# Kernel tuning notes

Measured on AMD Instinct MI355X. Metric: run time of the kernel, lower is better.

The kernel has to match this reference:

```python
import jax, jax.numpy as jnp
import numpy as np

B, N, D, H, C = 4, 1024, 768, 12, 3
Dh = D // H                      # 64
HID = int(D * 4.0 * (2.0 / 3.0)) # 2048 (SwiGLU hidden)
EPS = 1e-5


def layernorm(x, g, b):
    m = jnp.mean(x, axis=-1, keepdims=True)
    v = jnp.mean(jnp.square(x - m), axis=-1, keepdims=True)
    return (x - m) * jax.lax.rsqrt(v + EPS) * g + b


def setup_inputs() -> dict:
    key = jax.random.key(0)
    ks = jax.random.split(key, 8)
    x = jax.random.normal(ks[0], (B, N, D), jnp.float32)
    coords = jax.random.uniform(ks[1], (B, N, C), jnp.float32)
    qkv_w = jax.random.normal(ks[2], (3 * D, D), jnp.float32) * 0.02
    qkv_b = jnp.zeros((3 * D,), jnp.float32)
    rel_w = jax.random.normal(ks[3], (H, C), jnp.float32) * 0.1
    ln1_g = jnp.ones((D,), jnp.float32)
    ln1_b = jnp.zeros((D,), jnp.float32)
    ln2_g = jnp.ones((D,), jnp.float32)
    ln2_b = jnp.zeros((D,), jnp.float32)
    win_w = jax.random.normal(ks[4], (2 * HID, D), jnp.float32) * 0.02
    win_b = jnp.zeros((2 * HID,), jnp.float32)
    wout_w = jax.random.normal(ks[5], (D, HID), jnp.float32) * 0.02
    wout_b = jnp.zeros((D,), jnp.float32)
    return dict(x=x, coords=coords, ln1_g=ln1_g, ln1_b=ln1_b, qkv_w=qkv_w,
                qkv_b=qkv_b, rel_w=rel_w, ln2_g=ln2_g, ln2_b=ln2_b,
                win_w=win_w, win_b=win_b, wout_w=wout_w, wout_b=wout_b)


def reference(x, coords, ln1_g, ln1_b, qkv_w, qkv_b, rel_w, ln2_g, ln2_b,
              win_w, win_b, wout_w, wout_b):
    # --- PatchAttention on norm1(x) ---
    h = layernorm(x, ln1_g, ln1_b)
    qkv = h @ qkv_w.T + qkv_b                    # (B,N,3D)
    q, k, v = jnp.split(qkv, 3, axis=-1)

    def heads(t):  # (B,N,D) -> (B,H,N,Dh)
        return t.reshape(B, N, H, Dh).transpose(0, 2, 1, 3)

    qh, kh, vh = heads(q), heads(k), heads(v)
    scale = 1.0 / np.sqrt(Dh).astype(np.float32)
    scores = jnp.einsum('bhid,bhjd->bhij', qh, kh) * scale
    # coord bias: (coords_i - coords_j) . W_h  ==  p[b,h,i] - p[b,h,j]
    p = jnp.einsum('bnc,hc->bhn', coords, rel_w)  # (B,H,N)
    scores = scores + p[:, :, :, None] - p[:, :, None, :]
    attn = jax.nn.softmax(scores, axis=-1)
    o = jnp.einsum('bhij,bhjd->bhid', attn, vh)   # (B,H,N,Dh)
    o = o.transpose(0, 2, 1, 3).reshape(B, N, D)
    x = x + o

    # --- SwiGLU FFN on norm2(x) ---
    h2 = layernorm(x, ln2_g, ln2_b)
    uv = h2 @ win_w.T + win_b                     # (B,N,2*HID)
    u, g = jnp.split(uv, 2, axis=-1)
    act = jax.nn.silu(u) * g
    return x + act @ wout_w.T + wout_b
```

## Files before the change

kernel.cpp:

```cpp
#include <hip/hip_runtime.h>
#include <math.h>

typedef unsigned short u16;
typedef __bf16 bf16x8 __attribute__((ext_vector_type(8)));
typedef __bf16 bf16x4 __attribute__((ext_vector_type(4)));
typedef u16 u16x4 __attribute__((ext_vector_type(4)));
typedef float f32x4 __attribute__((ext_vector_type(4)));

#define NTOK 1024
#define DMODEL 768
#define NHEAD 12
#define LD3 2304
#define HIDDIM 2048

__device__ __forceinline__ float b2f(u16 u) {
  unsigned int t = ((unsigned int)u) << 16;
  float f;
  __builtin_memcpy(&f, &t, 4);
  return f;
}
__device__ __forceinline__ u16 f2b(float f) {
  unsigned int t;
  __builtin_memcpy(&t, &f, 4);
  t += 0x7fffu + ((t >> 16) & 1u);
  return (u16)(t >> 16);
}

__device__ __forceinline__ void gl_lds16(const u16* g, u16* l) {
  __builtin_amdgcn_global_load_lds(
      (__attribute__((address_space(1))) const unsigned int*)g,
      (__attribute__((address_space(3))) unsigned int*)l, 16, 0, 0);
}

__global__ __launch_bounds__(256) void signal_kernel(float* __restrict__ out,
                                                     int n, float c) {
  int i = blockIdx.x * 256 + threadIdx.x;
  if (i < n) out[i] = c;
}

struct CanonJobs {
  const void* s[13];
  u16* d[13];
  int n[13];
};

__global__ __launch_bounds__(256) void canon_kernel(CanonJobs jobs) {
  __shared__ int csh;
  u16 v = ((const u16*)jobs.s[0])[2 * threadIdx.x];
  int e = (v >> 7) & 0xFF;
  unsigned long long m = __ballot(e >= 0xC0);
  if (threadIdx.x == 0) csh = 0;
  __syncthreads();
  if ((threadIdx.x & 63) == 0) atomicAdd(&csh, __popcll(m));
  __syncthreads();
  bool isf32 = csh >= 8;

  int j = blockIdx.y;
  int n4 = jobs.n[j] >> 2;
  const void* s = jobs.s[j];
  u16* d = jobs.d[j];
  for (int i = blockIdx.x * 256 + threadIdx.x; i < n4; i += gridDim.x * 256) {
    if (isf32) {
      f32x4 vv = *((const f32x4*)s + i);
      u16x4 o = {f2b(vv[0]), f2b(vv[1]), f2b(vv[2]), f2b(vv[3])};
      *((u16x4*)d + i) = o;
    } else {
      *((u16x4*)d + i) = *((const u16x4*)s + i);
    }
  }
}

__global__ __launch_bounds__(256) void ln_bf16_kernel(
    const u16* __restrict__ x, const u16* __restrict__ g,
    const u16* __restrict__ b, u16* __restrict__ out) {
  int row = blockIdx.x;
  int tid = threadIdx.x;
  const u16* xr = x + (size_t)row * DMODEL;
  float v0 = b2f(xr[tid]), v1 = b2f(xr[tid + 256]), v2 = b2f(xr[tid + 512]);
  float s = v0 + v1 + v2;
  float q = v0 * v0 + v1 * v1 + v2 * v2;
#pragma unroll
  for (int off = 32; off; off >>= 1) {
    s += __shfl_xor(s, off, 64);
    q += __shfl_xor(q, off, 64);
  }
  __shared__ float rs[4], rq[4];
  int wv = tid >> 6;
  if ((tid & 63) == 0) { rs[wv] = s; rq[wv] = q; }
  __syncthreads();
  s = rs[0] + rs[1] + rs[2] + rs[3];
  q = rq[0] + rq[1] + rq[2] + rq[3];
  float mean = s * (1.0f / 768.0f);
  float var = q * (1.0f / 768.0f) - mean * mean;
  float inv = rsqrtf(var + 1e-5f);
  u16* outr = out + (size_t)row * DMODEL;
  outr[tid]       = f2b((v0 - mean) * inv * b2f(g[tid])       + b2f(b[tid]));
  outr[tid + 256] = f2b((v1 - mean) * inv * b2f(g[tid + 256]) + b2f(b[tid + 256]));
  outr[tid + 512] = f2b((v2 - mean) * inv * b2f(g[tid + 512]) + b2f(b[tid + 512]));
}

__global__ __launch_bounds__(256) void ln_f32_kernel(
    const float* __restrict__ x, const u16* __restrict__ g,
    const u16* __restrict__ b, u16* __restrict__ out) {
  int row = blockIdx.x;
  int tid = threadIdx.x;
  const float* xr = x + (size_t)row * DMODEL;
  float v0 = xr[tid], v1 = xr[tid + 256], v2 = xr[tid + 512];
  float s = v0 + v1 + v2;
  float q = v0 * v0 + v1 * v1 + v2 * v2;
#pragma unroll
  for (int off = 32; off; off >>= 1) {
    s += __shfl_xor(s, off, 64);
    q += __shfl_xor(q, off, 64);
  }
  __shared__ float rs[4], rq[4];
  int wv = tid >> 6;
  if ((tid & 63) == 0) { rs[wv] = s; rq[wv] = q; }
  __syncthreads();
  s = rs[0] + rs[1] + rs[2] + rs[3];
  q = rq[0] + rq[1] + rq[2] + rq[3];
  float mean = s * (1.0f / 768.0f);
  float var = q * (1.0f / 768.0f) - mean * mean;
  float inv = rsqrtf(var + 1e-5f);
  u16* outr = out + (size_t)row * DMODEL;
  outr[tid]       = f2b((v0 - mean) * inv * b2f(g[tid])       + b2f(b[tid]));
  outr[tid + 256] = f2b((v1 - mean) * inv * b2f(g[tid + 256]) + b2f(b[tid + 256]));
  outr[tid + 512] = f2b((v2 - mean) * inv * b2f(g[tid + 512]) + b2f(b[tid + 512]));
}

__global__ __launch_bounds__(256) void gemm_bt(
    const u16* __restrict__ Ap, const u16* __restrict__ Wp,
    const u16* __restrict__ bias, u16* __restrict__ Cp, int Nn, int K) {
  __shared__ __align__(16) u16 Al[3 * 128 * 32], Bl[3 * 64 * 32];
  int lane = threadIdx.x & 63;
  int wv = threadIdx.x >> 6;
  int q16 = lane & 15, quad = lane >> 4;
  int mB0 = blockIdx.y * 128;
  int nB0 = blockIdx.x * 64;
  int mW = (wv >> 1) * 64, nW = (wv & 1) * 32;
  int srow = lane >> 2;
  int scol = ((lane & 3) ^ ((lane >> 3) & 3)) * 8;
  int sx8 = (quad ^ ((q16 >> 1) & 3)) * 8;
  int r0 = wv * 32 + srow, r1 = r0 + 16;
  int rb = wv * 16 + srow;
  const u16* Ag0 = Ap + (size_t)(mB0 + r0) * K + scol;
  const u16* Ag1 = Ap + (size_t)(mB0 + r1) * K + scol;
  const u16* Wg  = Wp + (size_t)(nB0 + rb) * K + scol;
  int ch0 = wv * 1024, ch1 = ch0 + 512, chb = wv * 512;
  int nsteps = K >> 5;
  f32x4 acc[4][2] = {};
#pragma unroll
  for (int tt = 0; tt < 2; ++tt) {
    int k0 = tt * 32;
    gl_lds16(Ag0 + k0, Al + tt * 4096 + ch0);
    gl_lds16(Ag1 + k0, Al + tt * 4096 + ch1);
    gl_lds16(Wg + k0, Bl + tt * 2048 + chb);
  }
  int n3 = nsteps / 3;
  for (int kb = 0; kb < n3; ++kb) {
#pragma unroll
    for (int c = 0; c < 3; ++c) {
      int t = kb * 3 + c;
      if (t < nsteps - 1) asm volatile("s_waitcnt vmcnt(3)" ::: "memory");
      else                asm volatile("s_waitcnt vmcnt(0)" ::: "memory");
      __builtin_amdgcn_sched_barrier(0);
      __builtin_amdgcn_s_barrier();
      __builtin_amdgcn_sched_barrier(0);
      if (t < nsteps - 2) {
        int k0 = (t + 2) * 32;
        int bs = (c + 2) % 3;
        gl_lds16(Ag0 + k0, Al + bs * 4096 + ch0);
        gl_lds16(Ag1 + k0, Al + bs * 4096 + ch1);
        gl_lds16(Wg + k0, Bl + bs * 2048 + chb);
      }
      const __bf16* Ab = (const __bf16*)(Al + c * 4096);
      const __bf16* Bb = (const __bf16*)(Bl + c * 2048);
      bf16x8 af[4], bfr[2];
#pragma unroll
      for (int si = 0; si < 4; ++si)
        af[si] = *(const bf16x8*)(Ab + (mW + si * 16 + q16) * 32 + sx8);
#pragma unroll
      for (int sj = 0; sj < 2; ++sj)
        bfr[sj] = *(const bf16x8*)(Bb + (nW + sj * 16 + q16) * 32 + sx8);
#pragma unroll
      for (int si = 0; si < 4; ++si)
#pragma unroll
        for (int sj = 0; sj < 2; ++sj)
          acc[si][sj] = __builtin_amdgcn_mfma_f32_16x16x32_bf16(af[si], bfr[sj], acc[si][sj], 0, 0, 0);
    }
  }
#pragma unroll
  for (int si = 0; si < 4; ++si)
#pragma unroll
    for (int sj = 0; sj < 2; ++sj) {
      int col = nB0 + nW + sj * 16 + q16;
      float bcol = b2f(bias[col]);
#pragma unroll
      for (int r = 0; r < 4; ++r) {
        int rowi = mB0 + mW + si * 16 + quad * 4 + r;
        Cp[(size_t)rowi * Nn + col] = f2b(acc[si][sj][r] + bcol);
      }
    }
}

__global__ __launch_bounds__(256) void gemm_out_f32(
    const u16* __restrict__ Ap, const u16* __restrict__ Wp,
    const u16* __restrict__ bias, const float* __restrict__ res,
    float* __restrict__ out) {
  __shared__ __align__(16) u16 Al[4 * 64 * 32], Bl[4 * 64 * 32];
  int lane = threadIdx.x & 63;
  int wv = threadIdx.x >> 6;
  int q16 = lane & 15, quad = lane >> 4;
  int mB0 = blockIdx.y * 64;
  int nB0 = blockIdx.x * 64;
  int mW = (wv >> 1) * 32, nW = (wv & 1) * 32;
  int srow = lane >> 2;
  int scol = ((lane & 3) ^ ((lane >> 3) & 3)) * 8;
  int sx8 = (quad ^ ((q16 >> 1) & 3)) * 8;
  int ra = wv * 16 + srow;
  const u16* Ag = Ap + (size_t)(mB0 + ra) * 2048 + scol;
  const u16* Wg = Wp + (size_t)(nB0 + ra) * 2048 + scol;
  int ch = wv * 512;
  f32x4 acc[2][2] = {};
#pragma unroll
  for (int tt = 0; tt < 3; ++tt) {
    gl_lds16(Ag + tt * 32, Al + tt * 2048 + ch);
    gl_lds16(Wg + tt * 32, Bl + tt * 2048 + ch);
  }
  for (int kb = 0; kb < 16; ++kb) {
#pragma unroll
    for (int c = 0; c < 4; ++c) {
      int t = kb * 4 + c;
      if (t < 62)       asm volatile("s_waitcnt vmcnt(4)" ::: "memory");
      else if (t == 62) asm volatile("s_waitcnt vmcnt(2)" ::: "memory");
      else              asm volatile("s_waitcnt vmcnt(0)" ::: "memory");
      __builtin_amdgcn_sched_barrier(0);
      __builtin_amdgcn_s_barrier();
      __builtin_amdgcn_sched_barrier(0);
      if (t < 61) {
        int k0 = (t + 3) * 32;
        int bs = (c + 3) & 3;
        gl_lds16(Ag + k0, Al + bs * 2048 + ch);
        gl_lds16(Wg + k0, Bl + bs * 2048 + ch);
      }
      const __bf16* Ab = (const __bf16*)(Al + c * 2048);
      const __bf16* Bb = (const __bf16*)(Bl + c * 2048);
      bf16x8 af[2], bfr[2];
#pragma unroll
      for (int si = 0; si < 2; ++si)
        af[si] = *(const bf16x8*)(Ab + (mW + si * 16 + q16) * 32 + sx8);
#pragma unroll
      for (int sj = 0; sj < 2; ++sj)
        bfr[sj] = *(const bf16x8*)(Bb + (nW + sj * 16 + q16) * 32 + sx8);
#pragma unroll
      for (int si = 0; si < 2; ++si)
#pragma unroll
        for (int sj = 0; sj < 2; ++sj)
          acc[si][sj] = __builtin_amdgcn_mfma_f32_16x16x32_bf16(af[si], bfr[sj], acc[si][sj], 0, 0, 0);
    }
  }
#pragma unroll
  for (int si = 0; si < 2; ++si)
#pragma unroll
    for (int sj = 0; sj < 2; ++sj) {
      int col = nB0 + nW + sj * 16 + q16;
      float bcol = b2f(bias[col]);
#pragma unroll
      for (int r = 0; r < 4; ++r) {
        int rowi = mB0 + mW + si * 16 + quad * 4 + r;
        size_t idx = (size_t)rowi * 768 + col;
        out[idx] = acc[si][sj][r] + bcol + res[idx];
      }
    }
}

__global__ __launch_bounds__(256) void ffn_in_kernel(
    const u16* __restrict__ hp, const u16* __restrict__ Wp,
    const u16* __restrict__ bias, u16* __restrict__ actp) {
  __shared__ __align__(16) u16 Al[6 * 128 * 32], Bl[6 * 64 * 32];
  int lane = threadIdx.x & 63;
  int wv = threadIdx.x >> 6;
  int q16 = lane & 15, quad = lane >> 4;
  int mB0 = blockIdx.y * 128;
  int cB0 = blockIdx.x * 32;
  int mW = (wv >> 1) * 64;
  int cW = (wv & 1) * 16;
  int srow = lane >> 2;
  int scol = ((lane & 3) ^ ((lane >> 3) & 3)) * 8;
  int sx8 = (quad ^ ((q16 >> 1) & 3)) * 8;
  int r0 = wv * 32 + srow, r1 = r0 + 16;
  int rb = wv * 16 + srow;
  int gb = (rb < 32) ? (cB0 + rb) : (HIDDIM + cB0 + rb - 32);
  const u16* Ag0 = hp + (size_t)(mB0 + r0) * DMODEL + scol;
  const u16* Ag1 = hp + (size_t)(mB0 + r1) * DMODEL + scol;
  const u16* Wg  = Wp + (size_t)gb * DMODEL + scol;
  int ch0 = wv * 1024, ch1 = ch0 + 512, chb = wv * 512;
  f32x4 au[4] = {}, ag[4] = {};
#pragma unroll
  for (int tt = 0; tt < 5; ++tt) {
    int k0 = tt * 32;
    gl_lds16(Ag0 + k0, Al + tt * 4096 + ch0);
    gl_lds16(Ag1 + k0, Al + tt * 4096 + ch1);
    gl_lds16(Wg + k0, Bl + tt * 2048 + chb);
  }
  for (int kb = 0; kb < 4; ++kb) {
#pragma unroll
    for (int c = 0; c < 6; ++c) {
      int t = kb * 6 + c;
      if (t < 20)       asm volatile("s_waitcnt vmcnt(12)" ::: "memory");
      else if (t == 20) asm volatile("s_waitcnt vmcnt(9)" ::: "memory");
      else if (t == 21) asm volatile("s_waitcnt vmcnt(6)" ::: "memory");
      else if (t == 22) asm volatile("s_waitcnt vmcnt(3)" ::: "memory");
      else              asm volatile("s_waitcnt vmcnt(0)" ::: "memory");
      __builtin_amdgcn_sched_barrier(0);
      __builtin_amdgcn_s_barrier();
      __builtin_amdgcn_sched_barrier(0);
      if (t < 19) {
        int k0 = (t + 5) * 32;
        int bs = (c + 5) % 6;
        gl_lds16(Ag0 + k0, Al + bs * 4096 + ch0);
        gl_lds16(Ag1 + k0, Al + bs * 4096 + ch1);
        gl_lds16(Wg + k0, Bl + bs * 2048 + chb);
      }
      const __bf16* Ab = (const __bf16*)(Al + c * 4096);
      const __bf16* Bb = (const __bf16*)(Bl + c * 2048);
      bf16x8 af[4], wu, wg;
#pragma unroll
      for (int si = 0; si < 4; ++si)
        af[si] = *(const bf16x8*)(Ab + (mW + si * 16 + q16) * 32 + sx8);
      wu = *(const bf16x8*)(Bb + (cW + q16) * 32 + sx8);
      wg = *(const bf16x8*)(Bb + (32 + cW + q16) * 32 + sx8);
#pragma unroll
      for (int si = 0; si < 4; ++si) {
        au[si] = __builtin_amdgcn_mfma_f32_16x16x32_bf16(af[si], wu, au[si], 0, 0, 0);
        ag[si] = __builtin_amdgcn_mfma_f32_16x16x32_bf16(af[si], wg, ag[si], 0, 0, 0);
      }
    }
  }
  int col = cB0 + cW + q16;
  float bu = b2f(bias[col]);
  float bg = b2f(bias[HIDDIM + col]);
#pragma unroll
  for (int si = 0; si < 4; ++si) {
#pragma unroll
    for (int r = 0; r < 4; ++r) {
      int rowi = mB0 + mW + si * 16 + quad * 4 + r;
      float u = au[si][r] + bu;
      float g = ag[si][r] + bg;
      float s = u / (1.0f + __expf(-u));
      actp[(size_t)rowi * HIDDIM + col] = f2b(s * g);
    }
  }
}

__global__ __launch_bounds__(256) void vt_kernel(const u16* __restrict__ qkvp,
                                                 u16* __restrict__ vtp,
                                                 const u16* __restrict__ coords,
                                                 const u16* __restrict__ relw,
                                                 float* __restrict__ p) {
  int blk = blockIdx.x;
  int b = blk / 192;
  int rem = blk % 192;
  int h = rem >> 4;
  int nt = rem & 15;
  int wv = threadIdx.x >> 6;
  int d = threadIdx.x & 63;
  int n0 = nt * 64 + wv * 16;
  const u16* src = qkvp + ((size_t)(b * NTOK) + n0) * LD3 + 2 * DMODEL + h * 64 + d;
  u16* dst = vtp + ((size_t)((b * NHEAD + h) * 64 + d)) * NTOK + n0;
#pragma unroll
  for (int c = 0; c < 2; ++c) {
    u16 buf[8] __attribute__((aligned(16)));
#pragma unroll
    for (int i = 0; i < 8; ++i) buf[i] = src[(size_t)(c * 8 + i) * LD3];
    *(uint4*)(dst + c * 8) = *(const uint4*)buf;
  }
  if (nt == 0) {
    const float LOG2E = 1.4426950408889634f;
    float w0 = b2f(relw[h * 3 + 0]), w1 = b2f(relw[h * 3 + 1]), w2 = b2f(relw[h * 3 + 2]);
    float* prow = p + (size_t)(b * NHEAD + h) * NTOK;
    for (int n = threadIdx.x; n < NTOK; n += 256) {
      int idx = b * NTOK + n;
      float c0 = b2f(coords[idx * 3 + 0]);
      float c1 = b2f(coords[idx * 3 + 1]);
      float c2 = b2f(coords[idx * 3 + 2]);
      prow[n] = (c0 * w0 + c1 * w1 + c2 * w2) * LOG2E;
    }
  }
}

__global__ __launch_bounds__(256) void attn_kernel(
    const u16* __restrict__ qkvp, const u16* __restrict__ vtp,
    const float* __restrict__ p2, const u16* __restrict__ xp,
    float* __restrict__ x1) {
  const __bf16* qb = (const __bf16*)qkvp;
  __shared__ __align__(16) u16 Kl[4][32 * 64];
  __shared__ __align__(16) u16 Vl[4][64 * 32];
  __shared__ __align__(16) u16 Pl[4][16][40];
  __shared__ __align__(16) float Pb[1024];
  int lane = threadIdx.x & 63;
  int wv = threadIdx.x >> 6;
  int hw = blockIdx.x;
  int g = hw % 48;
  int nt = hw / 48;
  int b = g / 12, h = g % 12;
  int i0 = (nt * 4 + wv) * 16;
  int q16 = lane & 15, quad = lane >> 4;

  const float scl2 = 0.125f * 1.4426950408889634f;

  const __bf16* qrow = qb + ((size_t)(b * NTOK) + i0 + q16) * LD3 + h * 64;
  bf16x8 bq0 = *(const bf16x8*)(qrow + quad * 8);
  bf16x8 bq1 = *(const bf16x8*)(qrow + 32 + quad * 8);

  const float* prow = p2 + (size_t)(b * NHEAD + h) * NTOK;

  int krw = wv * 8 + (lane >> 3);
  int ks  = (lane & 7) ^ (krw & 7);
  const u16* kg0 = qkvp + (size_t)(b * NTOK) * LD3 + DMODEL + h * 64 + ks * 8;
  int vrw = wv * 16 + (lane >> 2);
  int vs  = (lane & 3) ^ ((vrw >> 1) & 3);
  const u16* vg0 = vtp + ((size_t)((b * NHEAD + h) * 64 + vrw)) * NTOK + vs * 8;

  int kx0 = (quad ^ (q16 & 7)) << 3;
  int kx1 = ((4 | quad) ^ (q16 & 7)) << 3;
  int vx  = (quad ^ ((q16 >> 1) & 3)) << 3;

  float mrun = -1e30f, lsum = 0.f;
  f32x4 accO[4] = {};

  gl_lds16((const u16*)(prow + wv * 256 + lane * 4), (u16*)&Pb[wv * 256]);
#pragma unroll
  for (int tt = 0; tt < 3; ++tt) {
    gl_lds16(kg0 + (size_t)(tt * 32 + krw) * LD3, &Kl[tt][wv * 512]);
    gl_lds16(vg0 + tt * 32, &Vl[tt][wv * 512]);
  }

  for (int kb = 0; kb < 8; ++kb) {
#pragma unroll
    for (int c = 0; c < 4; ++c) {
      int t = kb * 4 + c;
      if (t < 30)       asm volatile("s_waitcnt vmcnt(4)" ::: "memory");
      else if (t == 30) asm volatile("s_waitcnt vmcnt(2)" ::: "memory");
      else              asm volatile("s_waitcnt vmcnt(0)" ::: "memory");
      __builtin_amdgcn_sched_barrier(0);
      __builtin_amdgcn_s_barrier();
      __builtin_amdgcn_sched_barrier(0);
      if (t < 29) {
        int j = (t + 3) * 32;
        gl_lds16(kg0 + (size_t)(j + krw) * LD3, &Kl[(c + 3) & 3][wv * 512]);
        gl_lds16(vg0 + j, &Vl[(c + 3) & 3][wv * 512]);
      }

      int j0 = t * 32;
      const __bf16* Kb = (const __bf16*)Kl[c];
      bf16x8 ka00 = *(const bf16x8*)(Kb + q16 * 64 + kx0);
      bf16x8 ka01 = *(const bf16x8*)(Kb + q16 * 64 + kx1);
      bf16x8 ka10 = *(const bf16x8*)(Kb + (16 + q16) * 64 + kx0);
      bf16x8 ka11 = *(const bf16x8*)(Kb + (16 + q16) * 64 + kx1);
      f32x4 st0 = {}, st1 = {};
      st0 = __builtin_amdgcn_mfma_f32_16x16x32_bf16(ka00, bq0, st0, 0, 0, 0);
      st0 = __builtin_amdgcn_mfma_f32_16x16x32_bf16(ka01, bq1, st0, 0, 0, 0);
      st1 = __builtin_amdgcn_mfma_f32_16x16x32_bf16(ka10, bq0, st1, 0, 0, 0);
      st1 = __builtin_amdgcn_mfma_f32_16x16x32_bf16(ka11, bq1, st1, 0, 0, 0);

      f32x4 pjl = *(const f32x4*)(&Pb[j0 + 4 * quad]);
      f32x4 pjh = *(const f32x4*)(&Pb[j0 + 16 + 4 * quad]);
      float sl[4], sh[4];
#pragma unroll
      for (int r = 0; r < 4; ++r) {
        sl[r] = st0[r] * scl2 - pjl[r];
        sh[r] = st1[r] * scl2 - pjh[r];
      }
      float lm = fmaxf(fmaxf(fmaxf(sl[0], sl[1]), fmaxf(sl[2], sl[3])),
                       fmaxf(fmaxf(sh[0], sh[1]), fmaxf(sh[2], sh[3])));
      lm = fmaxf(lm, __shfl_xor(lm, 16, 64));
      lm = fmaxf(lm, __shfl_xor(lm, 32, 64));
      float mn = fmaxf(mrun, lm);
      float alpha = exp2f(mrun - mn);
      mrun = mn;
      float pl[4], ph[4];
#pragma unroll
      for (int r = 0; r < 4; ++r) {
        pl[r] = exp2f(sl[r] - mn);
        ph[r] = exp2f(sh[r] - mn);
      }
      float ts = (pl[0] + pl[1]) + (pl[2] + pl[3]) +
                 (ph[0] + ph[1]) + (ph[2] + ph[3]);
      ts += __shfl_xor(ts, 16, 64);
      ts += __shfl_xor(ts, 32, 64);
      lsum = lsum * alpha + ts;

      bf16x4 w0 = {(__bf16)pl[0], (__bf16)pl[1], (__bf16)pl[2], (__bf16)pl[3]};
      bf16x4 w1 = {(__bf16)ph[0], (__bf16)ph[1], (__bf16)ph[2], (__bf16)ph[3]};
      *(bf16x4*)(&Pl[wv][q16][4 * quad]) = w0;
      *(bf16x4*)(&Pl[wv][q16][16 + 4 * quad]) = w1;
      bf16x8 ap = *(const bf16x8*)(&Pl[wv][q16][quad * 8]);

      const __bf16* Vb = (const __bf16*)Vl[c];
#pragma unroll
      for (int ds = 0; ds < 4; ++ds) {
        bf16x8 av = *(const bf16x8*)(Vb + (ds * 16 + q16) * 32 + vx);
        f32x4 cc = accO[ds];
#pragma unroll
        for (int r = 0; r < 4; ++r) cc[r] *= alpha;
        accO[ds] = __builtin_amdgcn_mfma_f32_16x16x32_bf16(av, ap, cc, 0, 0, 0);
      }
    }
  }

  float rl = 1.0f / lsum;
  size_t rowbase = ((size_t)(b * NTOK) + i0 + q16) * DMODEL + h * 64;
#pragma unroll
  for (int ds = 0; ds < 4; ++ds) {
    int d0 = ds * 16 + quad * 4;
    u16x4 xv = *(const u16x4*)(xp + rowbase + d0);
    f32x4 ov;
#pragma unroll
    for (int r = 0; r < 4; ++r) ov[r] = b2f(xv[r]) + accO[ds][r] * rl;
    *(f32x4*)(x1 + rowbase + d0) = ov;
  }
}

extern "C" void kernel_launch(void* const* d_in, const int* in_sizes, int n_in,
                              void* d_out, int out_size, void* d_ws, size_t ws_size,
                              hipStream_t stream) {
  static const int esz[13] = {3145728, 12288, 768, 768, 1769472, 2304, 36,
                              768, 768, 3145728, 4096, 1572864, 768};
  float sig = -1.f;
  if (n_in != 13) {
    sig = 6000.f + 100.f * (float)n_in;
  } else {
    for (int i = 0; i < 13; ++i)
      if (in_sizes[i] != esz[i]) { sig = 1000.f + 100.f * (float)i; break; }
  }
  if (sig < 0.f && ws_size < 57258496ULL) sig = 3000.f;
  if (sig < 0.f && out_size != 3145728) sig = 3100.f;
  if (sig >= 0.f) {
    signal_kernel<<<(out_size + 255) / 256, 256, 0, stream>>>((float*)d_out, out_size, sig);
    return;
  }

  char* ws = (char*)d_ws;
  u16*  cx      = (u16*)(ws + 256);
  u16*  cqkvw   = (u16*)(ws + 6291712);
  u16*  cwinw   = (u16*)(ws + 9830656);
  u16*  cwoutw  = (u16*)(ws + 16122112);
  u16*  ccoords = (u16*)(ws + 19267840);
  u16*  cln1g   = (u16*)(ws + 19292416);
  u16*  cln1b   = (u16*)(ws + 19293952);
  u16*  cqkvb   = (u16*)(ws + 19295488);
  u16*  crelw   = (u16*)(ws + 19300096);
  u16*  cln2g   = (u16*)(ws + 19300352);
  u16*  cln2b   = (u16*)(ws + 19301888);
  u16*  cwinb   = (u16*)(ws + 19303424);
  u16*  cwoutb  = (u16*)(ws + 19311616);
  u16*  h       = (u16*)(ws + 19313152);
  u16*  qkv     = (u16*)(ws + 25604608);
  float* pbuf   = (float*)(ws + 44478976);
  float* x1     = (float*)(ws + 44675584);
  u16*  act     = qkv;
  u16*  vt      = h;

  CanonJobs jobs;
  u16* dsts[13] = {cx, ccoords, cln1g, cln1b, cqkvw, cqkvb, crelw,
                   cln2g, cln2b, cwinw, cwinb, cwoutw, cwoutb};
  for (int i = 0; i < 13; ++i) {
    jobs.s[i] = d_in[i];
    jobs.d[i] = dsts[i];
    jobs.n[i] = in_sizes[i];
  }
  canon_kernel<<<dim3(768, 13), 256, 0, stream>>>(jobs);

  ln_bf16_kernel<<<4096, 256, 0, stream>>>(cx, cln1g, cln1b, h);
  gemm_bt<<<dim3(36, 32), 256, 0, stream>>>(h, cqkvw, cqkvb, qkv, 2304, 768);
  vt_kernel<<<768, 256, 0, stream>>>(qkv, vt, ccoords, crelw, pbuf);
  attn_kernel<<<768, 256, 0, stream>>>(qkv, vt, pbuf, cx, x1);
  ln_f32_kernel<<<4096, 256, 0, stream>>>(x1, cln2g, cln2b, h);
  ffn_in_kernel<<<dim3(64, 32), 256, 0, stream>>>(h, cwinw, cwinb, act);
  gemm_out_f32<<<dim3(12, 64), 256, 0, stream>>>(act, cwoutw, cwoutb, x1,
                                                 (float*)d_out);
}
```

Measured before the change: 287.2 us.

## Switch FFN GEMMs to double-buffered 64-wide K tiles and skip redundant softmax rescale

The output and FFN-input GEMMs drop their 4- and 6-stage 32-wide K pipelines in favour of two buffers of 64-wide K tiles with a new XOR swizzle. Each stage now waits for all loads to finish (vmcnt(0)) before its barrier. This halves the number of barriers and loop iterations, but it reduces prefetch depth and so hides less memory latency. The attention kernel adds a wave-uniform check and skips the running-max exp and accumulator rescale when no lane's max increases.

New measurement: 275.3 us. 4.1% less time.

```diff
diff --git a/kernel.cpp b/kernel.cpp
--- a/kernel.cpp
+++ b/kernel.cpp
@@ -207,56 +207,63 @@
     const u16* __restrict__ Ap, const u16* __restrict__ Wp,
     const u16* __restrict__ bias, const float* __restrict__ res,
     float* __restrict__ out) {
-  __shared__ __align__(16) u16 Al[4 * 64 * 32], Bl[4 * 64 * 32];
+  __shared__ __align__(16) u16 Al[2 * 4096], Bl[2 * 4096];
   int lane = threadIdx.x & 63;
   int wv = threadIdx.x >> 6;
   int q16 = lane & 15, quad = lane >> 4;
   int mB0 = blockIdx.y * 64;
   int nB0 = blockIdx.x * 64;
   int mW = (wv >> 1) * 32, nW = (wv & 1) * 32;
-  int srow = lane >> 2;
-  int scol = ((lane & 3) ^ ((lane >> 3) & 3)) * 8;
-  int sx8 = (quad ^ ((q16 >> 1) & 3)) * 8;
-  int ra = wv * 16 + srow;
-  const u16* Ag = Ap + (size_t)(mB0 + ra) * 2048 + scol;
-  const u16* Wg = Wp + (size_t)(nB0 + ra) * 2048 + scol;
-  int ch = wv * 512;
+  int lr = lane >> 3, ls = lane & 7;
+  int sg = (ls ^ lr) * 8;
+  int sx0 = (quad ^ (q16 & 7)) * 8;
+  int sx1 = ((4 | quad) ^ (q16 & 7)) * 8;
+  const u16* Ag = Ap + (size_t)(mB0 + wv * 16 + lr) * 2048 + sg;
+  const u16* Wg = Wp + (size_t)(nB0 + wv * 16 + lr) * 2048 + sg;
+  int ch = wv * 1024;
   f32x4 acc[2][2] = {};
 #pragma unroll
-  for (int tt = 0; tt < 3; ++tt) {
-    gl_lds16(Ag + tt * 32, Al + tt * 2048 + ch);
-    gl_lds16(Wg + tt * 32, Bl + tt * 2048 + ch);
+  for (int i = 0; i < 2; ++i) {
+    gl_lds16(Ag + (size_t)i * 8 * 2048, Al + ch + i * 512);
+    gl_lds16(Wg + (size_t)i * 8 * 2048, Bl + ch + i * 512);
   }
   for (int kb = 0; kb < 16; ++kb) {
 #pragma unroll
-    for (int c = 0; c < 4; ++c) {
-      int t = kb * 4 + c;
-      if (t < 62)       asm volatile("s_waitcnt vmcnt(4)" ::: "memory");
-      else if (t == 62) asm volatile("s_waitcnt vmcnt(2)" ::: "memory");
-      else              asm volatile("s_waitcnt vmcnt(0)" ::: "memory");
+    for (int c = 0; c < 2; ++c) {
+      int t = kb * 2 + c;
+      asm volatile("s_waitcnt vmcnt(0)" ::: "memory");
       __builtin_amdgcn_sched_barrier(0);
       __builtin_amdgcn_s_barrier();
       __builtin_amdgcn_sched_barrier(0);
-      if (t < 61) {
-        int k0 = (t + 3) * 32;
-        int bs = (c + 3) & 3;
-        gl_lds16(Ag + k0, Al + bs * 2048 + ch);
-        gl_lds16(Wg + k0, Bl + bs * 2048 + ch);
-      }
-      const __bf16* Ab = (const __bf16*)(Al + c * 2048);
-      const __bf16* Bb = (const __bf16*)(Bl + c * 2048);
-      bf16x8 af[2], bfr[2];
+      if (t < 31) {
+        int k0 = (t + 1) * 64;
+        int bs = c ^ 1;
+#pragma unroll
+        for (int i = 0; i < 2; ++i) {
+          gl_lds16(Ag + (size_t)i * 8 * 2048 + k0, Al + bs * 4096 + ch + i * 512);
+          gl_lds16(Wg + (size_t)i * 8 * 2048 + k0, Bl + bs * 4096 + ch + i * 512);
+        }
+      }
+      const __bf16* Ab = (const __bf16*)(Al + c * 4096);
+      const __bf16* Bb = (const __bf16*)(Bl + c * 4096);
+      bf16x8 a0[2], a1[2], b0[2], b1[2];
+#pragma unroll
+      for (int si = 0; si < 2; ++si) {
+        a0[si] = *(const bf16x8*)(Ab + (mW + si * 16 + q16) * 64 + sx0);
+        a1[si] = *(const bf16x8*)(Ab + (mW + si * 16 + q16) * 64 + sx1);
+      }
+#pragma unroll
+      for (int sj = 0; sj < 2; ++sj) {
+        b0[sj] = *(const bf16x8*)(Bb + (nW + sj * 16 + q16) * 64 + sx0);
+        b1[sj] = *(const bf16x8*)(Bb + (nW + sj * 16 + q16) * 64 + sx1);
+      }
 #pragma unroll
       for (int si = 0; si < 2; ++si)
-        af[si] = *(const bf16x8*)(Ab + (mW + si * 16 + q16) * 32 + sx8);
-#pragma unroll
-      for (int sj = 0; sj < 2; ++sj)
-        bfr[sj] = *(const bf16x8*)(Bb + (nW + sj * 16 + q16) * 32 + sx8);
-#pragma unroll
-      for (int si = 0; si < 2; ++si)
-#pragma unroll
-        for (int sj = 0; sj < 2; ++sj)
-          acc[si][sj] = __builtin_amdgcn_mfma_f32_16x16x32_bf16(af[si], bfr[sj], acc[si][sj], 0, 0, 0);
+#pragma unroll
+        for (int sj = 0; sj < 2; ++sj) {
+          acc[si][sj] = __builtin_amdgcn_mfma_f32_16x16x32_bf16(a0[si], b0[sj], acc[si][sj], 0, 0, 0);
+          acc[si][sj] = __builtin_amdgcn_mfma_f32_16x16x32_bf16(a1[si], b1[sj], acc[si][sj], 0, 0, 0);
+        }
     }
   }
 #pragma unroll
@@ -277,7 +284,7 @@
 __global__ __launch_bounds__(256) void ffn_in_kernel(
     const u16* __restrict__ hp, const u16* __restrict__ Wp,
     const u16* __restrict__ bias, u16* __restrict__ actp) {
-  __shared__ __align__(16) u16 Al[6 * 128 * 32], Bl[6 * 64 * 32];
+  __shared__ __align__(16) u16 Al[2 * 8192], Bl[2 * 4096];
   int lane = threadIdx.x & 63;
   int wv = threadIdx.x >> 6;
   int q16 = lane & 15, quad = lane >> 4;
@@ -285,55 +292,61 @@
   int cB0 = blockIdx.x * 32;
   int mW = (wv >> 1) * 64;
   int cW = (wv & 1) * 16;
-  int srow = lane >> 2;
-  int scol = ((lane & 3) ^ ((lane >> 3) & 3)) * 8;
-  int sx8 = (quad ^ ((q16 >> 1) & 3)) * 8;
-  int r0 = wv * 32 + srow, r1 = r0 + 16;
-  int rb = wv * 16 + srow;
-  int gb = (rb < 32) ? (cB0 + rb) : (HIDDIM + cB0 + rb - 32);
-  const u16* Ag0 = hp + (size_t)(mB0 + r0) * DMODEL + scol;
-  const u16* Ag1 = hp + (size_t)(mB0 + r1) * DMODEL + scol;
-  const u16* Wg  = Wp + (size_t)gb * DMODEL + scol;
-  int ch0 = wv * 1024, ch1 = ch0 + 512, chb = wv * 512;
+  int lr = lane >> 3, ls = lane & 7;
+  int sg = (ls ^ lr) * 8;
+  int sx0 = (quad ^ (q16 & 7)) * 8;
+  int sx1 = ((4 | quad) ^ (q16 & 7)) * 8;
+  const u16* Ag = hp + (size_t)(mB0 + wv * 32 + lr) * DMODEL + sg;
+  int rB0 = wv * 16 + lr, rB1 = rB0 + 8;
+  int gb0 = (rB0 < 32) ? (cB0 + rB0) : (HIDDIM + cB0 + rB0 - 32);
+  int gb1 = (rB1 < 32) ? (cB0 + rB1) : (HIDDIM + cB0 + rB1 - 32);
+  const u16* Wg0 = Wp + (size_t)gb0 * DMODEL + sg;
+  const u16* Wg1 = Wp + (size_t)gb1 * DMODEL + sg;
+  int chA = wv * 2048, chB = wv * 1024;
   f32x4 au[4] = {}, ag[4] = {};
 #pragma unroll
-  for (int tt = 0; tt < 5; ++tt) {
-    int k0 = tt * 32;
-    gl_lds16(Ag0 + k0, Al + tt * 4096 + ch0);
-    gl_lds16(Ag1 + k0, Al + tt * 4096 + ch1);
-    gl_lds16(Wg + k0, Bl + tt * 2048 + chb);
-  }
-  for (int kb = 0; kb < 4; ++kb) {
-#pragma unroll
-    for (int c = 0; c < 6; ++c) {
-      int t = kb * 6 + c;
-      if (t < 20)       asm volatile("s_waitcnt vmcnt(12)" ::: "memory");
-      else if (t == 20) asm volatile("s_waitcnt vmcnt(9)" ::: "memory");
-      else if (t == 21) asm volatile("s_waitcnt vmcnt(6)" ::: "memory");
-      else if (t == 22) asm volatile("s_waitcnt vmcnt(3)" ::: "memory");
-      else              asm volatile("s_waitcnt vmcnt(0)" ::: "memory");
+  for (int i = 0; i < 4; ++i)
+    gl_lds16(Ag + (size_t)i * 8 * DMODEL, Al + chA + i * 512);
+  gl_lds16(Wg0, Bl + chB);
+  gl_lds16(Wg1, Bl + chB + 512);
+  for (int kb = 0; kb < 6; ++kb) {
+#pragma unroll
+    for (int c = 0; c < 2; ++c) {
+      int t = kb * 2 + c;
+      asm volatile("s_waitcnt vmcnt(0)" ::: "memory");
       __builtin_amdgcn_sched_barrier(0);
       __builtin_amdgcn_s_barrier();
       __builtin_amdgcn_sched_barrier(0);
-      if (t < 19) {
-        int k0 = (t + 5) * 32;
-        int bs = (c + 5) % 6;
-        gl_lds16(Ag0 + k0, Al + bs * 4096 + ch0);
-        gl_lds16(Ag1 + k0, Al + bs * 4096 + ch1);
-        gl_lds16(Wg + k0, Bl + bs * 2048 + chb);
-      }
-      const __bf16* Ab = (const __bf16*)(Al + c * 4096);
-      const __bf16* Bb = (const __bf16*)(Bl + c * 2048);
-      bf16x8 af[4], wu, wg;
-#pragma unroll
-      for (int si = 0; si < 4; ++si)
-        af[si] = *(const bf16x8*)(Ab + (mW + si * 16 + q16) * 32 + sx8);
-      wu = *(const bf16x8*)(Bb + (cW + q16) * 32 + sx8);
-      wg = *(const bf16x8*)(Bb + (32 + cW + q16) * 32 + sx8);
+      if (t < 11) {
+        int k0 = (t + 1) * 64;
+        int bs = c ^ 1;
+#pragma unroll
+        for (int i = 0; i < 4; ++i)
+          gl_lds16(Ag + (size_t)i * 8 * DMODEL + k0, Al + bs * 8192 + chA + i * 512);
+        gl_lds16(Wg0 + k0, Bl + bs * 4096 + chB);
+        gl_lds16(Wg1 + k0, Bl + bs * 4096 + chB + 512);
+      }
+      const __bf16* Ab = (const __bf16*)(Al + c * 8192);
+      const __bf16* Bb = (const __bf16*)(Bl + c * 4096);
+      bf16x8 a0[4], a1[4];
 #pragma unroll
       for (int si = 0; si < 4; ++si) {
-        au[si] = __builtin_amdgcn_mfma_f32_16x16x32_bf16(af[si], wu, au[si], 0, 0, 0);
-        ag[si] = __builtin_amdgcn_mfma_f32_16x16x32_bf16(af[si], wg, ag[si], 0, 0, 0);
+        a0[si] = *(const bf16x8*)(Ab + (mW + si * 16 + q16) * 64 + sx0);
+        a1[si] = *(const bf16x8*)(Ab + (mW + si * 16 + q16) * 64 + sx1);
+      }
+      bf16x8 wu0 = *(const bf16x8*)(Bb + (cW + q16) * 64 + sx0);
+      bf16x8 wu1 = *(const bf16x8*)(Bb + (cW + q16) * 64 + sx1);
+      bf16x8 wg0 = *(const bf16x8*)(Bb + (32 + cW + q16) * 64 + sx0);
+      bf16x8 wg1 = *(const bf16x8*)(Bb + (32 + cW + q16) * 64 + sx1);
+#pragma unroll
+      for (int si = 0; si < 4; ++si) {
+        au[si] = __builtin_amdgcn_mfma_f32_16x16x32_bf16(a0[si], wu0, au[si], 0, 0, 0);
+        ag[si] = __builtin_amdgcn_mfma_f32_16x16x32_bf16(a0[si], wg0, ag[si], 0, 0, 0);
+      }
+#pragma unroll
+      for (int si = 0; si < 4; ++si) {
+        au[si] = __builtin_amdgcn_mfma_f32_16x16x32_bf16(a1[si], wu1, au[si], 0, 0, 0);
+        ag[si] = __builtin_amdgcn_mfma_f32_16x16x32_bf16(a1[si], wg1, ag[si], 0, 0, 0);
       }
     }
   }
@@ -476,20 +489,24 @@
                        fmaxf(fmaxf(sh[0], sh[1]), fmaxf(sh[2], sh[3])));
       lm = fmaxf(lm, __shfl_xor(lm, 16, 64));
       lm = fmaxf(lm, __shfl_xor(lm, 32, 64));
-      float mn = fmaxf(mrun, lm);
-      float alpha = exp2f(mrun - mn);
-      mrun = mn;
+      int up = !__all(lm <= mrun);
+      float alpha = 1.f;
+      if (up) {
+        float mn = fmaxf(mrun, lm);
+        alpha = exp2f(mrun - mn);
+        mrun = mn;
+      }
       float pl[4], ph[4];
 #pragma unroll
       for (int r = 0; r < 4; ++r) {
-        pl[r] = exp2f(sl[r] - mn);
-        ph[r] = exp2f(sh[r] - mn);
+        pl[r] = exp2f(sl[r] - mrun);
+        ph[r] = exp2f(sh[r] - mrun);
       }
       float ts = (pl[0] + pl[1]) + (pl[2] + pl[3]) +
                  (ph[0] + ph[1]) + (ph[2] + ph[3]);
       ts += __shfl_xor(ts, 16, 64);
       ts += __shfl_xor(ts, 32, 64);
-      lsum = lsum * alpha + ts;
+      lsum = up ? (lsum * alpha + ts) : (lsum + ts);
 
       bf16x4 w0 = {(__bf16)pl[0], (__bf16)pl[1], (__bf16)pl[2], (__bf16)pl[3]};
       bf16x4 w1 = {(__bf16)ph[0], (__bf16)ph[1], (__bf16)ph[2], (__bf16)ph[3]};
@@ -502,8 +519,10 @@
       for (int ds = 0; ds < 4; ++ds) {
         bf16x8 av = *(const bf16x8*)(Vb + (ds * 16 + q16) * 32 + vx);
         f32x4 cc = accO[ds];
-#pragma unroll
-        for (int r = 0; r < 4; ++r) cc[r] *= alpha;
+        if (up) {
+#pragma unroll
+          for (int r = 0; r < 4; ++r) cc[r] *= alpha;
+        }
         accO[ds] = __builtin_amdgcn_mfma_f32_16x16x32_bf16(av, ap, cc, 0, 0, 0);
       }
     }
```
